# Performance work log

Hardware: AMD Instinct MI355X
Metric: run time of the kernel (lower is better)

## Reference

```python
import jax, jax.numpy as jnp
import numpy as np

P = 16          # patch size
GH = GW = 29    # grid (464/16)
N = GH * GW     # 841 tokens
E = 384         # embed dim
NH = 6          # heads
HD = E // NH    # 64
DEPTH = 8
EPS = 1e-5


def _dist_bias():
    g = jnp.linspace(0.0, 1.0, GH)
    gy, gx = jnp.meshgrid(g, g, indexing='ij')
    coords = jnp.stack([gy.ravel(), gx.ravel()], axis=-1)        # [N,2]
    d2 = ((coords[None, :, :] - coords[:, None, :]) ** 2).sum(-1)  # [N,N]
    return -d2 / d2.max()                                        # in [-1,0]


def _ln(x, g, b):
    m = x.mean(-1, keepdims=True)
    v = ((x - m) ** 2).mean(-1, keepdims=True)
    return (x - m) * jax.lax.rsqrt(v + EPS) * g + b


def _shift(x, dy, dx):
    # zero-pad shift, matching F.pad default 'constant' mode in the source
    B, C, H, W = x.shape
    if dy > 0:
        x = jnp.pad(x, ((0, 0), (0, 0), (dy, 0), (0, 0)))[:, :, :H, :]
    elif dy < 0:
        x = jnp.pad(x, ((0, 0), (0, 0), (0, -dy), (0, 0)))[:, :, -H:, :]
    if dx > 0:
        x = jnp.pad(x, ((0, 0), (0, 0), (0, 0), (dx, 0)))[:, :, :, :W]
    elif dx < 0:
        x = jnp.pad(x, ((0, 0), (0, 0), (0, 0), (0, -dx)))[:, :, :, -W:]
    return x


def _patchify(x):
    B, C, H, W = x.shape
    gh, gw = H // P, W // P
    x = x.reshape(B, C, gh, P, gw, P)
    x = x.transpose(0, 2, 4, 1, 3, 5)         # [B,gh,gw,C,p,p]
    return x.reshape(B, gh * gw, C * P * P)


def setup_inputs() -> dict:
    key = jax.random.key(0)
    ks = jax.random.split(key, 8)
    D = DEPTH
    s = 0.02
    inp = {
        'x': jax.random.normal(ks[0], (16, 3, 464, 464), jnp.float32),
        'tok_ng': jnp.ones((3840,), jnp.float32),
        'tok_nb': jnp.zeros((3840,), jnp.float32),
        'tok_w1': jax.random.normal(ks[1], (3840, 768), jnp.float32) * s,
        'tok_b1': jnp.zeros((768,), jnp.float32),
        'tok_w2': jax.random.normal(ks[2], (768, 384), jnp.float32) * s,
        'tok_b2': jnp.zeros((384,), jnp.float32),
        'ln1_g': jnp.ones((D, E), jnp.float32),
        'ln1_b': jnp.zeros((D, E), jnp.float32),
        'w_qkv': jax.random.normal(ks[3], (D, E, 3 * E), jnp.float32) * s,
        'temp': jnp.full((D, NH), np.log(HD ** -0.5), jnp.float32),
        'loc_w': jnp.full((D, NH), 0.1, jnp.float32),
        'w_proj': jax.random.normal(ks[4], (D, E, E), jnp.float32) * s,
        'b_proj': jnp.zeros((D, E), jnp.float32),
        'ls1': jnp.full((D, E), 1e-4, jnp.float32),
        'ln2_g': jnp.ones((D, E), jnp.float32),
        'ln2_b': jnp.zeros((D, E), jnp.float32),
        'ff_w1': jax.random.normal(ks[5], (D, E, 4 * E), jnp.float32) * s,
        'ff_b1': jnp.zeros((D, 4 * E), jnp.float32),
        'ff_w2': jax.random.normal(ks[6], (D, 4 * E, E), jnp.float32) * s,
        'ff_b2': jnp.zeros((D, E), jnp.float32),
        'ls2': jnp.full((D, E), 1e-4, jnp.float32),
    }
    return inp


def _forward(x, tok_ng, tok_nb, tok_w1, tok_b1, tok_w2, tok_b2,
             ln1_g, ln1_b, w_qkv, temp, loc_w, w_proj, b_proj, ls1,
             ln2_g, ln2_b, ff_w1, ff_b1, ff_w2, ff_b2, ls2):
    p2 = P // 2
    shifts = [x, _shift(x, p2, 0), _shift(x, -p2, 0), _shift(x, 0, p2), _shift(x, 0, -p2)]
    patches = jnp.concatenate([_patchify(s) for s in shifts], axis=-1)  # [B,N,3840]
    h = _ln(patches, tok_ng, tok_nb)
    h = jax.nn.gelu(h @ tok_w1 + tok_b1, approximate=False)
    h = h @ tok_w2 + tok_b2                                             # [B,N,E]

    loc = _dist_bias()                                                  # [N,N]

    def block(h, p):
        (g1, b1, wqkv, tp, lw, wp, bp, l1, g2, b2, fw1, fb1, fw2, fb2, l2) = p
        y = _ln(h, g1, b1)
        qkv = (y @ wqkv).reshape(h.shape[0], N, 3, NH, HD)
        qkv = qkv.transpose(2, 0, 3, 1, 4)                              # [3,B,H,N,hd]
        q, k, v = qkv[0], qkv[1], qkv[2]
        scale = jnp.exp(tp)[:, None, None]                              # per-head temperature
        logits = jnp.einsum('bhnd,bhmd->bhnm', q, k) * scale
        logits = logits + lw[:, None, None] * loc                       # per-head locality bias
        a = jax.nn.softmax(logits, axis=-1)
        o = jnp.einsum('bhnm,bhmd->bhnd', a, v)
        o = o.transpose(0, 2, 1, 3).reshape(h.shape[0], N, E)
        h = h + l1 * (o @ wp + bp)
        y2 = _ln(h, g2, b2)
        f = jax.nn.gelu(y2 @ fw1 + fb1, approximate=False) @ fw2 + fb2
        h = h + l2 * f
        return h, None

    params = (ln1_g, ln1_b, w_qkv, temp, loc_w, w_proj, b_proj, ls1,
              ln2_g, ln2_b, ff_w1, ff_b1, ff_w2, ff_b2, ls2)
    h, _ = jax.lax.scan(block, h, params)
    return h


def reference(x, tok_ng, tok_nb, tok_w1, tok_b1, tok_w2, tok_b2,
              ln1_g, ln1_b, w_qkv, temp, loc_w, w_proj, b_proj, ls1,
              ln2_g, ln2_b, ff_w1, ff_b1, ff_w2, ff_b2, ls2):
    return _forward(x, tok_ng, tok_nb, tok_w1, tok_b1, tok_w2, tok_b2,
                    ln1_g, ln1_b, w_qkv, temp, loc_w, w_proj, b_proj, ls1,
                    ln2_g, ln2_b, ff_w1, ff_b1, ff_w2, ff_b2, ls2)
```

## Files before the change

### kernel.cpp

```cpp
#include <hip/hip_runtime.h>
#include <math.h>

typedef __attribute__((ext_vector_type(8))) short short8;
typedef __attribute__((ext_vector_type(4))) float f32x4;
typedef unsigned short u16;

#define NTOK 841
#define GRID_H 29
#define E_ 384
#define NH_ 6
#define MROWS 13456
#define MP 13568
#define MQ 14336
#define CM 5120

__device__ __forceinline__ u16 f2bf(float f) {
  union { float f; unsigned int u; } c; c.f = f;
  unsigned int u = c.u;
  return (u16)((u + 0x7fffu + ((u >> 16) & 1u)) >> 16);
}

__device__ __forceinline__ float bf2f(u16 b) {
  union { unsigned int u; float f; } c; c.u = ((unsigned int)b) << 16; return c.f;
}

__device__ __forceinline__ float gelu_exact(float v) {
  return 0.5f * v * (1.f + erff(v * 0.70710678118654752440f));
}

__device__ __forceinline__ float fexp2(float x) {
  float r; asm("v_exp_f32 %0, %1" : "=v"(r) : "v"(x)); return r;
}

__device__ __forceinline__ int swz64(int row, int col) {
  return row * 128 + ((((col >> 3) ^ (row & 7)) << 4) | ((col & 7) << 1));
}

__global__ __launch_bounds__(256) void transpose_conv(const float* __restrict__ in,
    u16* __restrict__ out, int K, int N) {
  __shared__ float tile[32][33];
  size_t zo = (size_t)blockIdx.z * K * N;
  const float* inp = in + zo;
  u16* outp = out + zo;
  int n0 = blockIdx.x * 32, k0 = blockIdx.y * 32;
  int tx = threadIdx.x & 31, ty = threadIdx.x >> 5;
  #pragma unroll
  for (int r = ty; r < 32; r += 8) tile[r][tx] = inp[(size_t)(k0 + r) * N + n0 + tx];
  __syncthreads();
  #pragma unroll
  for (int r = ty; r < 32; r += 8) outp[(size_t)(n0 + r) * K + k0 + tx] = f2bf(tile[tx][r]);
}

__global__ __launch_bounds__(256) void patch_ln(const float* __restrict__ x,
    const float* __restrict__ g, const float* __restrict__ bsh, u16* __restrict__ out,
    int t0) {
  int t = t0 + blockIdx.x;
  int tid = threadIdx.x;
  u16* orow = out + (size_t)blockIdx.x * 3840;
  if (t >= MROWS) {
    #pragma unroll
    for (int j = 0; j < 15; ++j) orow[tid + j * 256] = 0;
    return;
  }
  int bimg = t / NTOK, n = t % NTOK;
  int gy = n / GRID_H, gx = n % GRID_H;
  float vals[15];
  float s1 = 0.f, s2 = 0.f;
  #pragma unroll
  for (int j = 0; j < 15; ++j) {
    int cout = tid + j * 256;
    int s = cout / 768, rem = cout % 768;
    int c = rem / 256, rem2 = rem % 256;
    int py = rem2 / 16, px = rem2 % 16;
    int dy = (s == 1 ? 8 : 0) - (s == 2 ? 8 : 0);
    int dx = (s == 3 ? 8 : 0) - (s == 4 ? 8 : 0);
    int Y = gy * 16 + py - dy;
    int X = gx * 16 + px - dx;
    float v = 0.f;
    if (Y >= 0 && Y < 464 && X >= 0 && X < 464)
      v = x[(((size_t)bimg * 3 + c) * 464 + Y) * 464 + X];
    vals[j] = v;
    s1 += v; s2 += v * v;
  }
  #pragma unroll
  for (int m = 1; m < 64; m <<= 1) { s1 += __shfl_xor(s1, m); s2 += __shfl_xor(s2, m); }
  __shared__ float ws1[4], ws2[4];
  int wid = tid >> 6;
  if ((tid & 63) == 0) { ws1[wid] = s1; ws2[wid] = s2; }
  __syncthreads();
  s1 = ws1[0] + ws1[1] + ws1[2] + ws1[3];
  s2 = ws2[0] + ws2[1] + ws2[2] + ws2[3];
  float mean = s1 * (1.f / 3840.f);
  float var = s2 * (1.f / 3840.f) - mean * mean;
  float rs = rsqrtf(var + 1e-5f);
  #pragma unroll
  for (int j = 0; j < 15; ++j) {
    int cout = tid + j * 256;
    orow[cout] = f2bf((vals[j] - mean) * rs * g[cout] + bsh[cout]);
  }
}

__global__ __launch_bounds__(256) void ln384(const float* __restrict__ h,
    const float* __restrict__ g, const float* __restrict__ bsh, u16* __restrict__ y) {
  int row = blockIdx.x * 4 + (threadIdx.x >> 6);
  int lane = threadIdx.x & 63;
  const float* hr = h + (size_t)row * E_;
  float v[6];
  float s1 = 0.f;
  #pragma unroll
  for (int j = 0; j < 6; ++j) { v[j] = hr[lane + j * 64]; s1 += v[j]; }
  #pragma unroll
  for (int m = 1; m < 64; m <<= 1) s1 += __shfl_xor(s1, m);
  float mean = s1 * (1.f / 384.f);
  float s2 = 0.f;
  #pragma unroll
  for (int j = 0; j < 6; ++j) { float d = v[j] - mean; s2 += d * d; }
  #pragma unroll
  for (int m = 1; m < 64; m <<= 1) s2 += __shfl_xor(s2, m);
  float rs = rsqrtf(s2 * (1.f / 384.f) + 1e-5f);
  u16* yr = y + (size_t)row * E_;
  #pragma unroll
  for (int j = 0; j < 6; ++j) {
    int c = lane + j * 64;
    yr[c] = f2bf((v[j] - mean) * rs * g[c] + bsh[c]);
  }
}

__global__ __launch_bounds__(256) void ln384p(const float* __restrict__ h,
    const float* __restrict__ g, const float* __restrict__ bsh, u16* __restrict__ yp) {
  int rowp = blockIdx.x * 4 + (threadIdx.x >> 6);
  int lane = threadIdx.x & 63;
  int bg = rowp / 896, tk = rowp - bg * 896;
  u16* yr = yp + (size_t)rowp * E_;
  if (tk >= NTOK) {
    #pragma unroll
    for (int j = 0; j < 6; ++j) yr[lane + j * 64] = 0;
    return;
  }
  const float* hr = h + (size_t)(bg * NTOK + tk) * E_;
  float v[6];
  float s1 = 0.f;
  #pragma unroll
  for (int j = 0; j < 6; ++j) { v[j] = hr[lane + j * 64]; s1 += v[j]; }
  #pragma unroll
  for (int m = 1; m < 64; m <<= 1) s1 += __shfl_xor(s1, m);
  float mean = s1 * (1.f / 384.f);
  float s2 = 0.f;
  #pragma unroll
  for (int j = 0; j < 6; ++j) { float d = v[j] - mean; s2 += d * d; }
  #pragma unroll
  for (int m = 1; m < 64; m <<= 1) s2 += __shfl_xor(s2, m);
  float rs = rsqrtf(s2 * (1.f / 384.f) + 1e-5f);
  #pragma unroll
  for (int j = 0; j < 6; ++j) {
    int c = lane + j * 64;
    yr[c] = f2bf((v[j] - mean) * rs * g[c] + bsh[c]);
  }
}

template<int EPI, int TM, int BK>
__global__ __launch_bounds__(256) void gemm_bt(
    const u16* __restrict__ A, const u16* __restrict__ BT,
    int N, int K,
    const float* __restrict__ bias, const float* __restrict__ lscale,
    float* __restrict__ resid, u16* __restrict__ outb, float* __restrict__ outf) {
  constexpr int MI = TM / 32;
  constexpr int BUF = (TM + 128) * BK;
  constexpr int SM1 = 2 * BUF * 2;
  constexpr int SM2 = (EPI == 1) ? TM * 136 * 2 : 0;
  constexpr int SMEM = SM1 > SM2 ? SM1 : SM2;
  __shared__ alignas(16) char smem[SMEM];
  short* As = (short*)smem;
  const int gx = gridDim.x;
  const int nwg = gx * gridDim.y;
  int L = blockIdx.x + blockIdx.y * gx;
  int q8 = nwg >> 3, r8 = nwg & 7, xcd = L & 7, pos = L >> 3;
  int L2 = (xcd < r8 ? xcd * (q8 + 1) : r8 * (q8 + 1) + (xcd - r8) * q8) + pos;
  const int m0 = (L2 / gx) * TM, n0 = (L2 % gx) * 128;
  const int tid = threadIdx.x;
  const int lane = tid & 63, wid = tid >> 6;
  const int wm = wid >> 1, wn = wid & 1;
  f32x4 acc[MI][4] = {};
  const int nkt = K / BK;

  auto stage = [&](int b, int kt) {
    short* Ab = As + b * BUF;
    short* Bb = Ab + TM * BK;
    const int k0 = kt * BK;
    if constexpr (BK == 64) {
      const int rowl = lane >> 3;
      const int colc = (((lane & 7) ^ (rowl & 7)) << 3);
      #pragma unroll
      for (int i = 0; i < TM / 32; ++i) {
        int chunk = i * 4 + wid;
        const u16* ga = A + (size_t)(m0 + chunk * 8 + rowl) * K + k0 + colc;
        __builtin_amdgcn_global_load_lds((const __attribute__((address_space(1))) void*)ga,
            (__attribute__((address_space(3))) void*)(Ab + (chunk << 9)), 16, 0, 0);
      }
      #pragma unroll
      for (int i = 0; i < 4; ++i) {
        int chunk = i * 4 + wid;
        const u16* gb = BT + (size_t)(n0 + chunk * 8 + rowl) * K + k0 + colc;
        __builtin_amdgcn_global_load_lds((const __attribute__((address_space(1))) void*)gb,
            (__attribute__((address_space(3))) void*)(Bb + (chunk << 9)), 16, 0, 0);
      }
    } else {
      const int rowl = lane >> 2;
      const int colc = (((lane & 3) ^ (rowl & 3)) << 3);
      #pragma unroll
      for (int i = 0; i < TM / 64; ++i) {
        int rbase = i * 64 + wid * 16;
        const u16* ga = A + (size_t)(m0 + rbase + rowl) * K + k0 + colc;
        __builtin_amdgcn_global_load_lds((const __attribute__((address_space(1))) void*)ga,
            (__attribute__((address_space(3))) void*)(Ab + rbase * 32), 16, 0, 0);
      }
      #pragma unroll
      for (int i = 0; i < 2; ++i) {
        int rbase = i * 64 + wid * 16;
        const u16* gb = BT + (size_t)(n0 + rbase + rowl) * K + k0 + colc;
        __builtin_amdgcn_global_load_lds((const __attribute__((address_space(1))) void*)gb,
            (__attribute__((address_space(3))) void*)(Bb + rbase * 32), 16, 0, 0);
      }
    }
  };

  const int lg = lane >> 4;
  stage(0, 0);
  for (int kt = 0; kt < nkt; ++kt) {
    const int cur = kt & 1;
    if (kt + 1 < nkt) {
      stage(cur ^ 1, kt + 1);
      if constexpr (BK == 64) {
        if constexpr (TM == 128) asm volatile("s_waitcnt vmcnt(8)" ::: "memory");
        else                     asm volatile("s_waitcnt vmcnt(6)" ::: "memory");
      } else {
        if constexpr (TM == 128) asm volatile("s_waitcnt vmcnt(4)" ::: "memory");
        else                     asm volatile("s_waitcnt vmcnt(3)" ::: "memory");
      }
    } else {
      asm volatile("s_waitcnt vmcnt(0)" ::: "memory");
    }
    __builtin_amdgcn_s_barrier();
    __builtin_amdgcn_sched_barrier(0);
    short* Ab = As + cur * BUF;
    short* Bb = Ab + TM * BK;
    #pragma unroll
    for (int kk = 0; kk < BK / 32; ++kk) {
      short8 a[MI], bfr[4];
      #pragma unroll
      for (int mi = 0; mi < MI; ++mi) {
        int ra = wm * (TM / 2) + mi * 16 + (lane & 15);
        int off = (BK == 64) ? ((((kk << 2) | lg) ^ (ra & 7)) << 3)
                             : ((lg ^ (ra & 3)) << 3);
        a[mi] = *(const short8*)(Ab + ra * BK + off);
      }
      #pragma unroll
      for (int nj = 0; nj < 4; ++nj) {
        int rb = wn * 64 + nj * 16 + (lane & 15);
        int off = (BK == 64) ? ((((kk << 2) | lg) ^ (rb & 7)) << 3)
                             : ((lg ^ (rb & 3)) << 3);
        bfr[nj] = *(const short8*)(Bb + rb * BK + off);
      }
      #pragma unroll
      for (int mi = 0; mi < MI; ++mi)
        #pragma unroll
        for (int nj = 0; nj < 4; ++nj)
          acc[mi][nj] = __builtin_amdgcn_mfma_f32_16x16x32_bf16(a[mi], bfr[nj], acc[mi][nj], 0, 0, 0);
    }
    __builtin_amdgcn_s_barrier();
  }
  const int rrow = (lane >> 4) << 2;
  const int ccol = lane & 15;
  if (EPI == 1) {
    u16* Cs = (u16*)smem;
    __syncthreads();
    #pragma unroll
    for (int mi = 0; mi < MI; ++mi)
      #pragma unroll
      for (int nj = 0; nj < 4; ++nj) {
        int cc = wn * 64 + nj * 16 + ccol;
        float bi = bias[n0 + cc];
        #pragma unroll
        for (int r = 0; r < 4; ++r) {
          int cr = wm * (TM / 2) + mi * 16 + rrow + r;
          Cs[cr * 136 + cc] = f2bf(gelu_exact(acc[mi][nj][r] + bi));
        }
      }
    __syncthreads();
    #pragma unroll
    for (int it = 0; it < TM / 16; ++it) {
      int idx = it * 256 + tid;
      int orow = idx >> 4, c = idx & 15;
      short8 v = *(const short8*)(Cs + orow * 136 + c * 8);
      *(short8*)(outb + (size_t)(m0 + orow) * N + n0 + c * 8) = v;
    }
    return;
  }
  #pragma unroll
  for (int mi = 0; mi < MI; ++mi)
    #pragma unroll
    for (int nj = 0; nj < 4; ++nj) {
      int gn = n0 + wn * 64 + nj * 16 + ccol;
      #pragma unroll
      for (int r = 0; r < 4; ++r) {
        int gm = m0 + wm * (TM / 2) + mi * 16 + rrow + r;
        float v = acc[mi][nj][r];
        if (EPI == 2) {
          outf[(size_t)gm * N + gn] = v + bias[gn];
        } else if (EPI == 3) {
          float* p = resid + (size_t)gm * N + gn;
          *p = *p + lscale[gn] * (v + bias[gn]);
        } else {
          if (gm < MROWS)
            outf[(size_t)gm * N + gn] =
                resid[(size_t)gm * N + gn] + lscale[gn] * (v + bias[gn]);
        }
      }
    }
}

__global__ __launch_bounds__(256) void gemm_qkv(
    const u16* __restrict__ A, const u16* __restrict__ BT,
    u16* __restrict__ Qp, u16* __restrict__ Kp, u16* __restrict__ Vp) {
  const int K = 384;
  constexpr int BUF = 256 * 32;
  constexpr int SM1 = 2 * BUF * 2;
  constexpr int SM2 = 128 * 136 * 2;
  constexpr int SMEM = SM1 > SM2 ? SM1 : SM2;
  __shared__ alignas(16) char smem[SMEM];
  short* As = (short*)smem;
  int L = blockIdx.x + blockIdx.y * 9;
  int L2 = (L & 7) * 126 + (L >> 3);
  const int m0 = (L2 / 9) * 128, n0 = (L2 % 9) * 128;
  const int tid = threadIdx.x;
  const int lane = tid & 63, wid = tid >> 6;
  const int wm = wid >> 1, wn = wid & 1;
  f32x4 acc[4][4] = {};

  auto stage = [&](int b, int kt) {
    short* Ab = As + b * BUF;
    short* Bb = Ab + 128 * 32;
    const int k0 = kt * 32;
    const int rowl = lane >> 2;
    const int colc = (((lane & 3) ^ (rowl & 3)) << 3);
    #pragma unroll
    for (int i = 0; i < 2; ++i) {
      int rbase = i * 64 + wid * 16;
      const u16* ga = A + (size_t)(m0 + rbase + rowl) * K + k0 + colc;
      __builtin_amdgcn_global_load_lds((const __attribute__((address_space(1))) void*)ga,
          (__attribute__((address_space(3))) void*)(Ab + rbase * 32), 16, 0, 0);
      const u16* gb = BT + (size_t)(n0 + rbase + rowl) * K + k0 + colc;
      __builtin_amdgcn_global_load_lds((const __attribute__((address_space(1))) void*)gb,
          (__attribute__((address_space(3))) void*)(Bb + rbase * 32), 16, 0, 0);
    }
  };

  const int lg = lane >> 4;
  stage(0, 0);
  for (int kt = 0; kt < 12; ++kt) {
    const int cur = kt & 1;
    if (kt + 1 < 12) {
      stage(cur ^ 1, kt + 1);
      asm volatile("s_waitcnt vmcnt(4)" ::: "memory");
    } else {
      asm volatile("s_waitcnt vmcnt(0)" ::: "memory");
    }
    __builtin_amdgcn_s_barrier();
    __builtin_amdgcn_sched_barrier(0);
    short* Ab = As + cur * BUF;
    short* Bb = Ab + 128 * 32;
    short8 a[4], bfr[4];
    #pragma unroll
    for (int mi = 0; mi < 4; ++mi) {
      int ra = wm * 64 + mi * 16 + (lane & 15);
      a[mi] = *(const short8*)(Ab + ra * 32 + ((lg ^ (ra & 3)) << 3));
    }
    #pragma unroll
    for (int nj = 0; nj < 4; ++nj) {
      int rb = wn * 64 + nj * 16 + (lane & 15);
      bfr[nj] = *(const short8*)(Bb + rb * 32 + ((lg ^ (rb & 3)) << 3));
    }
    #pragma unroll
    for (int mi = 0; mi < 4; ++mi)
      #pragma unroll
      for (int nj = 0; nj < 4; ++nj)
        acc[mi][nj] = __builtin_amdgcn_mfma_f32_16x16x32_bf16(a[mi], bfr[nj], acc[mi][nj], 0, 0, 0);
    __builtin_amdgcn_s_barrier();
  }
  const int seg = n0 / 384;
  const int h0 = (n0 - seg * 384) >> 6;
  const int bg = m0 / 896;
  const int tk0 = m0 - bg * 896;
  const int rrow = (lane >> 4) << 2;
  const int ccol = lane & 15;
  u16* Cs = (u16*)smem;
  __syncthreads();
  #pragma unroll
  for (int mi = 0; mi < 4; ++mi)
    #pragma unroll
    for (int nj = 0; nj < 4; ++nj) {
      int cc = wn * 64 + nj * 16 + ccol;
      #pragma unroll
      for (int r = 0; r < 4; ++r) {
        int cr = wm * 64 + mi * 16 + rrow + r;
        u16 bv = f2bf(acc[mi][nj][r]);
        if (seg == 2) Cs[cc * 136 + cr] = bv;
        else          Cs[cr * 136 + cc] = bv;
      }
    }
  __syncthreads();
  #pragma unroll
  for (int i = 0; i < 8; ++i) {
    int idx = i * 256 + tid;
    int c = idx & 7;
    int orow = idx >> 3;
    int hs = orow >> 7;
    int rl = orow & 127;
    size_t bh = (size_t)(bg * 6 + h0 + hs);
    if (seg == 2) {
      int tile_l = rl >> 6, hd = rl & 63;
      short8 v = *(const short8*)(Cs + (hs * 64 + hd) * 136 + tile_l * 64 + c * 8);
      int tile = (tk0 >> 6) + tile_l;
      *(short8*)(Vp + bh * 57344 + tile * 4096 + hd * 64 + ((c ^ (hd & 7)) << 3)) = v;
    } else {
      short8 v = *(const short8*)(Cs + rl * 136 + hs * 64 + c * 8);
      if (seg == 0) {
        *(short8*)(Qp + (bh * 896 + tk0 + rl) * 64 + c * 8) = v;
      } else {
        int tok = tk0 + rl;
        *(short8*)(Kp + bh * 57344 + (tok >> 6) * 4096 + (tok & 63) * 64 + ((c ^ (tok & 7)) << 3)) = v;
      }
    }
  }
}

__global__ __launch_bounds__(512) void attn_sp(const u16* __restrict__ Qp,
    const u16* __restrict__ Kp, const u16* __restrict__ Vp,
    const float* __restrict__ temp_d, const float* __restrict__ locw_d,
    u16* __restrict__ ob) {
  int Lw = blockIdx.x;
  int L2 = (Lw & 7) * 84 + (Lw >> 3);
  const int bh = L2 / 7, qp = L2 % 7;
  const int hh = bh % NH_;
  const int tid = threadIdx.x, lane = tid & 63, w = tid >> 6;
  const int lg = lane >> 4, lc = lane & 15;
  const float LOG2E = 1.44269504088896f;
  const float scale = __expf(temp_d[hh]) * LOG2E;
  const float lwh = locw_d[hh] * LOG2E * -0.5f;

  __shared__ alignas(16) char ktl[2][8192];
  __shared__ alignas(16) char vtl[2][8192];
  __shared__ alignas(16) char pl[8][2048];
  __shared__ float yx2[896 * 2];

  for (int j = tid; j < 896; j += 512) {
    unsigned jc = j < NTOK ? (unsigned)j : (NTOK - 1);
    yx2[j * 2]     = (float)(jc / 29u) * (1.f / 28.f);
    yx2[j * 2 + 1] = (float)(jc % 29u) * (1.f / 28.f);
  }

  const char* qb = (const char*)(Qp + ((size_t)bh * 896 + qp * 128) * 64);
  short8 qf0 = *(const short8*)(qb + (w * 16 + lc) * 128 + lg * 16);
  short8 qf1 = *(const short8*)(qb + (w * 16 + lc) * 128 + 64 + lg * 16);

  const char* kbase = (const char*)Kp + (size_t)bh * 14 * 8192;
  const char* vbase = (const char*)Vp + (size_t)bh * 14 * 8192;

  auto stage = [&](int b, int kt) {
    int off = w * 1024;
    __builtin_amdgcn_global_load_lds(
        (const __attribute__((address_space(1))) void*)(kbase + kt * 8192 + off + lane * 16),
        (__attribute__((address_space(3))) void*)(ktl[b] + off), 16, 0, 0);
    __builtin_amdgcn_global_load_lds(
        (const __attribute__((address_space(1))) void*)(vbase + kt * 8192 + off + lane * 16),
        (__attribute__((address_space(3))) void*)(vtl[b] + off), 16, 0, 0);
  };

  f32x4 of[4] = {};
  float mrow[4], psum[4];
  #pragma unroll
  for (int r = 0; r < 4; ++r) { mrow[r] = -3e38f; psum[r] = 0.f; }

  stage(0, 0);
  asm volatile("s_waitcnt vmcnt(0)" ::: "memory");
  __syncthreads();

  float qyw[4], qxw[4];
  #pragma unroll
  for (int r = 0; r < 4; ++r) {
    int iq = qp * 128 + w * 16 + (lg << 2) + r;
    qyw[r] = -2.f * lwh * yx2[iq * 2];
    qxw[r] = -2.f * lwh * yx2[iq * 2 + 1];
  }

  for (int kt = 0; kt < 14; ++kt) {
    const int b = kt & 1;
    if (kt < 13) stage(b ^ 1, kt + 1);

    const char* kb = ktl[b];
    const char* vb = vtl[b];
    f32x4 sf[4];
    __builtin_amdgcn_s_setprio(1);
    #pragma unroll
    for (int nt = 0; nt < 4; ++nt) {
      short8 kf0 = *(const short8*)(kb + swz64(nt * 16 + lc, lg << 3));
      short8 kf1 = *(const short8*)(kb + swz64(nt * 16 + lc, 32 + (lg << 3)));
      f32x4 z = {0.f, 0.f, 0.f, 0.f};
      z = __builtin_amdgcn_mfma_f32_16x16x32_bf16(qf0, kf0, z, 0, 0, 0);
      z = __builtin_amdgcn_mfma_f32_16x16x32_bf16(qf1, kf1, z, 0, 0, 0);
      sf[nt] = z;
    }
    __builtin_amdgcn_s_setprio(0);

    const int jb = kt * 64;
    #pragma unroll
    for (int nt = 0; nt < 4; ++nt) {
      int j = jb + nt * 16 + lc;
      float jy = yx2[j * 2], jx = yx2[j * 2 + 1];
      float bc = lwh * (jy * jy + jx * jx);
      #pragma unroll
      for (int r = 0; r < 4; ++r) {
        float val = sf[nt][r] * scale + bc;
        val += qyw[r] * jy;
        val += qxw[r] * jx;
        sf[nt][r] = val;
      }
    }
    if (jb + 64 > NTOK) {
      #pragma unroll
      for (int nt = 0; nt < 4; ++nt) {
        if (jb + nt * 16 + lc >= NTOK) {
          sf[nt][0] = -3e38f; sf[nt][1] = -3e38f; sf[nt][2] = -3e38f; sf[nt][3] = -3e38f;
        }
      }
    }

    float lm[4];
    #pragma unroll
    for (int r = 0; r < 4; ++r)
      lm[r] = fmaxf(fmaxf(sf[0][r], sf[1][r]), fmaxf(sf[2][r], sf[3][r]));
    bool trig = (lm[0] > mrow[0] + 12.f) | (lm[1] > mrow[1] + 12.f) |
                (lm[2] > mrow[2] + 12.f) | (lm[3] > mrow[3] + 12.f);
    if (__any(trig)) {
      #pragma unroll
      for (int r = 0; r < 4; ++r) {
        float tm = lm[r];
        #pragma unroll
        for (int m = 1; m < 16; m <<= 1) tm = fmaxf(tm, __shfl_xor(tm, m));
        float mnew = fmaxf(mrow[r], tm);
        float alpha = fexp2(mrow[r] - mnew);
        psum[r] *= alpha;
        of[0][r] *= alpha; of[1][r] *= alpha; of[2][r] *= alpha; of[3][r] *= alpha;
        mrow[r] = mnew;
      }
    }

    char* plw = pl[w];
    #pragma unroll
    for (int nt = 0; nt < 4; ++nt) {
      float p0 = fexp2(sf[nt][0] - mrow[0]);
      float p1 = fexp2(sf[nt][1] - mrow[1]);
      float p2 = fexp2(sf[nt][2] - mrow[2]);
      float p3 = fexp2(sf[nt][3] - mrow[3]);
      psum[0] += p0; psum[1] += p1; psum[2] += p2; psum[3] += p3;
      unsigned w01, w23;
      asm("v_cvt_pk_bf16_f32 %0, %1, %2" : "=v"(w01) : "v"(p0), "v"(p1));
      asm("v_cvt_pk_bf16_f32 %0, %1, %2" : "=v"(w23) : "v"(p2), "v"(p3));
      int col = nt * 16 + lc;
      *(u16*)(plw + swz64((lg << 2) + 0, col)) = (u16)w01;
      *(u16*)(plw + swz64((lg << 2) + 1, col)) = (u16)(w01 >> 16);
      *(u16*)(plw + swz64((lg << 2) + 2, col)) = (u16)w23;
      *(u16*)(plw + swz64((lg << 2) + 3, col)) = (u16)(w23 >> 16);
    }
    asm volatile("s_waitcnt lgkmcnt(0)" ::: "memory");
    __builtin_amdgcn_sched_barrier(0);
    short8 pa[2];
    #pragma unroll
    for (int t = 0; t < 2; ++t)
      pa[t] = *(const short8*)(plw + swz64(lc, t * 32 + (lg << 3)));

    __builtin_amdgcn_s_setprio(1);
    #pragma unroll
    for (int n2 = 0; n2 < 4; ++n2) {
      f32x4 accv = of[n2];
      #pragma unroll
      for (int t = 0; t < 2; ++t) {
        short8 vf = *(const short8*)(vb + swz64(n2 * 16 + lc, t * 32 + (lg << 3)));
        accv = __builtin_amdgcn_mfma_f32_16x16x32_bf16(pa[t], vf, accv, 0, 0, 0);
      }
      of[n2] = accv;
    }
    __builtin_amdgcn_s_setprio(0);

    if (kt < 13) {
      asm volatile("s_waitcnt vmcnt(0) lgkmcnt(0)" ::: "memory");
      __builtin_amdgcn_sched_barrier(0);
      __builtin_amdgcn_s_barrier();
    }
  }

  const int bimg = bh / NH_;
  #pragma unroll
  for (int r = 0; r < 4; ++r) {
    float s = psum[r];
    #pragma unroll
    for (int m = 1; m < 16; m <<= 1) s += __shfl_xor(s, m);
    int iq = qp * 128 + w * 16 + (lg << 2) + r;
    if (iq < NTOK) {
      float rl = 1.f / s;
      #pragma unroll
      for (int n2 = 0; n2 < 4; ++n2)
        ob[((size_t)(bimg * NTOK + iq)) * E_ + hh * 64 + n2 * 16 + lc] =
            f2bf(of[n2][r] * rl);
    }
  }
}

extern "C" void kernel_launch(void* const* d_in, const int* in_sizes, int n_in,
                              void* d_out, int out_size, void* d_ws, size_t ws_size,
                              hipStream_t stream) {
  const float* x      = (const float*)d_in[0];
  const float* tok_ng = (const float*)d_in[1];
  const float* tok_nb = (const float*)d_in[2];
  const float* tok_w1 = (const float*)d_in[3];
  const float* tok_b1 = (const float*)d_in[4];
  const float* tok_w2 = (const float*)d_in[5];
  const float* tok_b2 = (const float*)d_in[6];
  const float* ln1_g  = (const float*)d_in[7];
  const float* ln1_b  = (const float*)d_in[8];
  const float* w_qkv  = (const float*)d_in[9];
  const float* temp   = (const float*)d_in[10];
  const float* loc_w  = (const float*)d_in[11];
  const float* w_proj = (const float*)d_in[12];
  const float* b_proj = (const float*)d_in[13];
  const float* ls1    = (const float*)d_in[14];
  const float* ln2_g  = (const float*)d_in[15];
  const float* ln2_b  = (const float*)d_in[16];
  const float* ff_w1  = (const float*)d_in[17];
  const float* ff_b1  = (const float*)d_in[18];
  const float* ff_w2  = (const float*)d_in[19];
  const float* ff_b2  = (const float*)d_in[20];
  const float* ls2    = (const float*)d_in[21];
  float* out = (float*)d_out;

  char* ws = (char*)d_ws;
  size_t off = 0;
  auto alloc = [&](size_t bytes) -> void* {
    void* p = ws + off; off += (bytes + 255) & ~(size_t)255; return p;
  };
  u16* w1T   = (u16*)alloc(768UL * 3840 * 2);
  u16* w2T   = (u16*)alloc(384UL * 768 * 2);
  u16* qkvT  = (u16*)alloc(8UL * 1152 * 384 * 2);
  u16* projT = (u16*)alloc(8UL * 384 * 384 * 2);
  u16* f1T   = (u16*)alloc(8UL * 1536 * 384 * 2);
  u16* f2T   = (u16*)alloc(8UL * 384 * 1536 * 2);
  float* h   = (float*)alloc((size_t)MP * 384 * 4);
  char* regB = (char*)alloc(22500000);
  u16* h1   = (u16*)regB;
  u16* ypad = (u16*)regB;
  u16* yff  = (u16*)regB;
  u16* ob   = (u16*)(regB + 11010048);
  char* regA = (char*)alloc((size_t)MP * 1536 * 2);
  u16* Xlnc = (u16*)regA;
  u16* Qp   = (u16*)regA;
  u16* Kp   = (u16*)(regA + 11010048);
  u16* Vp   = (u16*)(regA + 22020096);
  u16* f1b  = (u16*)regA;
  (void)in_sizes; (void)n_in; (void)out_size;

  if (off > ws_size) return;

  transpose_conv<<<dim3(24, 120, 1), 256, 0, stream>>>(tok_w1, w1T, 3840, 768);
  transpose_conv<<<dim3(12, 24, 1), 256, 0, stream>>>(tok_w2, w2T, 768, 384);
  transpose_conv<<<dim3(36, 12, 8), 256, 0, stream>>>(w_qkv, qkvT, 384, 1152);
  transpose_conv<<<dim3(12, 12, 8), 256, 0, stream>>>(w_proj, projT, 384, 384);
  transpose_conv<<<dim3(48, 12, 8), 256, 0, stream>>>(ff_w1, f1T, 384, 1536);
  transpose_conv<<<dim3(12, 48, 8), 256, 0, stream>>>(ff_w2, f2T, 1536, 384);

  for (int m = 0; m < MP; m += CM) {
    int rows = MP - m; if (rows > CM) rows = CM;
    patch_ln<<<rows, 256, 0, stream>>>(x, tok_ng, tok_nb, Xlnc, m);
    gemm_bt<1, 64, 64><<<dim3(6, rows / 64), 256, 0, stream>>>(Xlnc, w1T, 768, 3840,
        tok_b1, nullptr, nullptr, h1 + (size_t)m * 768, nullptr);
  }
  gemm_bt<2, 64, 64><<<dim3(3, MP / 64), 256, 0, stream>>>(h1, w2T, 384, 768, tok_b2,
      nullptr, nullptr, nullptr, h);

  for (int d = 0; d < 8; ++d) {
    ln384p<<<MQ / 4, 256, 0, stream>>>(h, ln1_g + d * E_, ln1_b + d * E_, ypad);
    gemm_qkv<<<dim3(9, 112), 256, 0, stream>>>(ypad, qkvT + (size_t)d * 1152 * 384, Qp, Kp, Vp);
    attn_sp<<<672, 512, 0, stream>>>(Qp, Kp, Vp, temp + d * NH_, loc_w + d * NH_, ob);
    gemm_bt<3, 64, 64><<<dim3(3, MP / 64), 256, 0, stream>>>(ob, projT + (size_t)d * 384 * 384,
        384, 384, b_proj + d * E_, ls1 + d * E_, h, nullptr, nullptr);
    ln384<<<MP / 4, 256, 0, stream>>>(h, ln2_g + d * E_, ln2_b + d * E_, yff);
    gemm_bt<1, 128, 32><<<dim3(12, MP / 128), 256, 0, stream>>>(yff, f1T + (size_t)d * 1536 * 384,
        1536, 384, ff_b1 + d * 1536, nullptr, nullptr, f1b, nullptr);
    if (d < 7)
      gemm_bt<3, 64, 64><<<dim3(3, MP / 64), 256, 0, stream>>>(f1b, f2T + (size_t)d * 384 * 1536,
          384, 1536, ff_b2 + d * E_, ls2 + d * E_, h, nullptr, nullptr);
    else
      gemm_bt<4, 64, 64><<<dim3(3, MP / 64), 256, 0, stream>>>(f1b, f2T + (size_t)d * 384 * 1536,
          384, 1536, ff_b2 + d * E_, ls2 + d * E_, h, nullptr, out);
  }
}
```

Measured before the change: 1.599 ms.

## Transpose attention MFMA operands to keep P in registers via shuffles

```diff
diff --git a/kernel.cpp b/kernel.cpp
--- a/kernel.cpp
+++ b/kernel.cpp
@@ -434,7 +434,7 @@
   }
 }
 
-__global__ __launch_bounds__(512) void attn_sp(const u16* __restrict__ Qp,
+__global__ __launch_bounds__(512, 8) void attn_sp(const u16* __restrict__ Qp,
     const u16* __restrict__ Kp, const u16* __restrict__ Vp,
     const float* __restrict__ temp_d, const float* __restrict__ locw_d,
     u16* __restrict__ ob) {
@@ -450,7 +450,6 @@
 
   __shared__ alignas(16) char ktl[2][8192];
   __shared__ alignas(16) char vtl[2][8192];
-  __shared__ alignas(16) char pl[8][2048];
   __shared__ float yx2[896 * 2];
 
   for (int j = tid; j < 896; j += 512) {
@@ -477,21 +476,19 @@
   };
 
   f32x4 of[4] = {};
-  float mrow[4], psum[4];
-  #pragma unroll
-  for (int r = 0; r < 4; ++r) { mrow[r] = -3e38f; psum[r] = 0.f; }
+  float mrow = -3e38f, psum = 0.f;
 
   stage(0, 0);
   asm volatile("s_waitcnt vmcnt(0)" ::: "memory");
   __syncthreads();
 
-  float qyw[4], qxw[4];
-  #pragma unroll
-  for (int r = 0; r < 4; ++r) {
-    int iq = qp * 128 + w * 16 + (lg << 2) + r;
-    qyw[r] = -2.f * lwh * yx2[iq * 2];
-    qxw[r] = -2.f * lwh * yx2[iq * 2 + 1];
-  }
+  const int iq = qp * 128 + w * 16 + lc;
+  const float qyw = -2.f * lwh * yx2[iq * 2];
+  const float qxw = -2.f * lwh * yx2[iq * 2 + 1];
+
+  const int src0 = ((lane & 16) << 1) + lc;
+  const int src1 = src0 + 16;
+  const bool hi = (lane >= 32);
 
   for (int kt = 0; kt < 14; ++kt) {
     const int b = kt & 1;
@@ -506,8 +503,8 @@
       short8 kf0 = *(const short8*)(kb + swz64(nt * 16 + lc, lg << 3));
       short8 kf1 = *(const short8*)(kb + swz64(nt * 16 + lc, 32 + (lg << 3)));
       f32x4 z = {0.f, 0.f, 0.f, 0.f};
-      z = __builtin_amdgcn_mfma_f32_16x16x32_bf16(qf0, kf0, z, 0, 0, 0);
-      z = __builtin_amdgcn_mfma_f32_16x16x32_bf16(qf1, kf1, z, 0, 0, 0);
+      z = __builtin_amdgcn_mfma_f32_16x16x32_bf16(kf0, qf0, z, 0, 0, 0);
+      z = __builtin_amdgcn_mfma_f32_16x16x32_bf16(kf1, qf1, z, 0, 0, 0);
       sf[nt] = z;
     }
     __builtin_amdgcn_s_setprio(0);
@@ -515,69 +512,70 @@
     const int jb = kt * 64;
     #pragma unroll
     for (int nt = 0; nt < 4; ++nt) {
-      int j = jb + nt * 16 + lc;
-      float jy = yx2[j * 2], jx = yx2[j * 2 + 1];
-      float bc = lwh * (jy * jy + jx * jx);
+      const float* cp = yx2 + (jb + nt * 16 + (lg << 2)) * 2;
+      f32x4 cA = *(const f32x4*)cp;
+      f32x4 cB = *(const f32x4*)(cp + 4);
       #pragma unroll
       for (int r = 0; r < 4; ++r) {
-        float val = sf[nt][r] * scale + bc;
-        val += qyw[r] * jy;
-        val += qxw[r] * jx;
-        sf[nt][r] = val;
+        float jy = (r < 2) ? cA[(r & 1) * 2] : cB[(r & 1) * 2];
+        float jx = (r < 2) ? cA[(r & 1) * 2 + 1] : cB[(r & 1) * 2 + 1];
+        float bc = lwh * (jy * jy + jx * jx);
+        sf[nt][r] = sf[nt][r] * scale + bc + qyw * jy + qxw * jx;
       }
     }
     if (jb + 64 > NTOK) {
       #pragma unroll
-      for (int nt = 0; nt < 4; ++nt) {
-        if (jb + nt * 16 + lc >= NTOK) {
-          sf[nt][0] = -3e38f; sf[nt][1] = -3e38f; sf[nt][2] = -3e38f; sf[nt][3] = -3e38f;
-        }
-      }
-    }
-
-    float lm[4];
-    #pragma unroll
-    for (int r = 0; r < 4; ++r)
-      lm[r] = fmaxf(fmaxf(sf[0][r], sf[1][r]), fmaxf(sf[2][r], sf[3][r]));
-    bool trig = (lm[0] > mrow[0] + 12.f) | (lm[1] > mrow[1] + 12.f) |
-                (lm[2] > mrow[2] + 12.f) | (lm[3] > mrow[3] + 12.f);
-    if (__any(trig)) {
-      #pragma unroll
-      for (int r = 0; r < 4; ++r) {
-        float tm = lm[r];
+      for (int nt = 0; nt < 4; ++nt)
         #pragma unroll
-        for (int m = 1; m < 16; m <<= 1) tm = fmaxf(tm, __shfl_xor(tm, m));
-        float mnew = fmaxf(mrow[r], tm);
-        float alpha = fexp2(mrow[r] - mnew);
-        psum[r] *= alpha;
-        of[0][r] *= alpha; of[1][r] *= alpha; of[2][r] *= alpha; of[3][r] *= alpha;
-        mrow[r] = mnew;
-      }
-    }
-
-    char* plw = pl[w];
+        for (int r = 0; r < 4; ++r)
+          if (jb + nt * 16 + (lg << 2) + r >= NTOK) sf[nt][r] = -3e38f;
+    }
+
+    float lm = sf[0][0];
+    #pragma unroll
+    for (int nt = 0; nt < 4; ++nt)
+      #pragma unroll
+      for (int r = 0; r < 4; ++r) lm = fmaxf(lm, sf[nt][r]);
+    if (__any(lm > mrow + 12.f)) {
+      float tm = lm;
+      tm = fmaxf(tm, __shfl_xor(tm, 16));
+      tm = fmaxf(tm, __shfl_xor(tm, 32));
+      float mnew = fmaxf(mrow, tm);
+      float alpha = fexp2(mrow - mnew);
+      psum *= alpha;
+      #pragma unroll
+      for (int n2 = 0; n2 < 4; ++n2) {
+        of[n2][0] *= alpha; of[n2][1] *= alpha; of[n2][2] *= alpha; of[n2][3] *= alpha;
+      }
+      mrow = mnew;
+    }
+
+    unsigned Wp[4][2];
     #pragma unroll
     for (int nt = 0; nt < 4; ++nt) {
-      float p0 = fexp2(sf[nt][0] - mrow[0]);
-      float p1 = fexp2(sf[nt][1] - mrow[1]);
-      float p2 = fexp2(sf[nt][2] - mrow[2]);
-      float p3 = fexp2(sf[nt][3] - mrow[3]);
-      psum[0] += p0; psum[1] += p1; psum[2] += p2; psum[3] += p3;
-      unsigned w01, w23;
-      asm("v_cvt_pk_bf16_f32 %0, %1, %2" : "=v"(w01) : "v"(p0), "v"(p1));
-      asm("v_cvt_pk_bf16_f32 %0, %1, %2" : "=v"(w23) : "v"(p2), "v"(p3));
-      int col = nt * 16 + lc;
-      *(u16*)(plw + swz64((lg << 2) + 0, col)) = (u16)w01;
-      *(u16*)(plw + swz64((lg << 2) + 1, col)) = (u16)(w01 >> 16);
-      *(u16*)(plw + swz64((lg << 2) + 2, col)) = (u16)w23;
-      *(u16*)(plw + swz64((lg << 2) + 3, col)) = (u16)(w23 >> 16);
-    }
-    asm volatile("s_waitcnt lgkmcnt(0)" ::: "memory");
-    __builtin_amdgcn_sched_barrier(0);
+      float p0 = fexp2(sf[nt][0] - mrow);
+      float p1 = fexp2(sf[nt][1] - mrow);
+      float p2 = fexp2(sf[nt][2] - mrow);
+      float p3 = fexp2(sf[nt][3] - mrow);
+      psum += p0 + p1 + p2 + p3;
+      asm("v_cvt_pk_bf16_f32 %0, %1, %2" : "=v"(Wp[nt][0]) : "v"(p0), "v"(p1));
+      asm("v_cvt_pk_bf16_f32 %0, %1, %2" : "=v"(Wp[nt][1]) : "v"(p2), "v"(p3));
+    }
+
     short8 pa[2];
     #pragma unroll
-    for (int t = 0; t < 2; ++t)
-      pa[t] = *(const short8*)(plw + swz64(lc, t * 32 + (lg << 3)));
+    for (int t = 0; t < 2; ++t) {
+      unsigned a0 = __shfl(Wp[2 * t][0], src0), a1 = __shfl(Wp[2 * t + 1][0], src0);
+      unsigned b0 = __shfl(Wp[2 * t][1], src0), b1 = __shfl(Wp[2 * t + 1][1], src0);
+      unsigned c0 = __shfl(Wp[2 * t][0], src1), c1 = __shfl(Wp[2 * t + 1][0], src1);
+      unsigned d0 = __shfl(Wp[2 * t][1], src1), d1 = __shfl(Wp[2 * t + 1][1], src1);
+      union { unsigned u[4]; short8 s; } pk;
+      pk.u[0] = hi ? a1 : a0;
+      pk.u[1] = hi ? b1 : b0;
+      pk.u[2] = hi ? c1 : c0;
+      pk.u[3] = hi ? d1 : d0;
+      pa[t] = pk.s;
+    }
 
     __builtin_amdgcn_s_setprio(1);
     #pragma unroll
@@ -586,7 +584,7 @@
       #pragma unroll
       for (int t = 0; t < 2; ++t) {
         short8 vf = *(const short8*)(vb + swz64(n2 * 16 + lc, t * 32 + (lg << 3)));
-        accv = __builtin_amdgcn_mfma_f32_16x16x32_bf16(pa[t], vf, accv, 0, 0, 0);
+        accv = __builtin_amdgcn_mfma_f32_16x16x32_bf16(vf, pa[t], accv, 0, 0, 0);
       }
       of[n2] = accv;
     }
@@ -600,18 +598,21 @@
   }
 
   const int bimg = bh / NH_;
-  #pragma unroll
-  for (int r = 0; r < 4; ++r) {
-    float s = psum[r];
-    #pragma unroll
-    for (int m = 1; m < 16; m <<= 1) s += __shfl_xor(s, m);
-    int iq = qp * 128 + w * 16 + (lg << 2) + r;
-    if (iq < NTOK) {
-      float rl = 1.f / s;
-      #pragma unroll
-      for (int n2 = 0; n2 < 4; ++n2)
-        ob[((size_t)(bimg * NTOK + iq)) * E_ + hh * 64 + n2 * 16 + lc] =
-            f2bf(of[n2][r] * rl);
+  float s = psum;
+  s += __shfl_xor(s, 16);
+  s += __shfl_xor(s, 32);
+  if (iq < NTOK) {
+    float rl = 1.f / s;
+    #pragma unroll
+    for (int n2 = 0; n2 < 4; ++n2) {
+      float v0 = of[n2][0] * rl, v1 = of[n2][1] * rl;
+      float v2 = of[n2][2] * rl, v3 = of[n2][3] * rl;
+      unsigned o01, o23;
+      asm("v_cvt_pk_bf16_f32 %0, %1, %2" : "=v"(o01) : "v"(v0), "v"(v1));
+      asm("v_cvt_pk_bf16_f32 %0, %1, %2" : "=v"(o23) : "v"(v2), "v"(v3));
+      u16* op = ob + ((size_t)(bimg * NTOK + iq)) * E_ + hh * 64 + n2 * 16 + (lg << 2);
+      *(unsigned*)op = o01;
+      *(unsigned*)(op + 2) = o23;
     }
   }
 }
```

Result: slower. 2.008 ms (+25.5%).
